# Kernel tuning notes

Hardware: AMD Instinct MI355X
Metric: run time of the kernel (lower is better)

Reference implementation:

```python
import jax, jax.numpy as jnp
import numpy as np

N_NODES = 50000
E_DIR = 250000
IN_FEATS = 256
N_HIDDEN = 64
N_CLASSES = 40
HEADS = 4
NEG_SLOPE = 0.2


def _build_graph():
    # mirrors to_undirected(edge_index) then add_self_loops(...)
    rng = np.random.default_rng(0)
    s = rng.integers(0, N_NODES, E_DIR)
    d = rng.integers(0, N_NODES, E_DIR)
    edges = np.stack([np.concatenate([s, d]), np.concatenate([d, s])], axis=0)
    edges = np.unique(edges, axis=1)  # dedup, as to_undirected does
    loops = np.arange(N_NODES)
    src = np.concatenate([edges[0], loops]).astype(np.int32)
    dst = np.concatenate([edges[1], loops]).astype(np.int32)
    return jnp.asarray(src), jnp.asarray(dst)


def setup_inputs() -> dict:
    key = jax.random.key(0)
    ks = jax.random.split(key, 16)
    src, dst = _build_graph()
    x = jax.random.uniform(ks[0], (N_NODES, IN_FEATS), dtype=jnp.float32)
    scale = 0.05
    # layer 0: IN -> HEADS*N_HIDDEN
    W0 = jax.random.normal(ks[1], (IN_FEATS, HEADS * N_HIDDEN), dtype=jnp.float32) * scale
    al0 = jax.random.normal(ks[2], (HEADS, N_HIDDEN), dtype=jnp.float32) * scale
    ar0 = jax.random.normal(ks[3], (HEADS, N_HIDDEN), dtype=jnp.float32) * scale
    b0 = jnp.zeros((HEADS * N_HIDDEN,), dtype=jnp.float32)
    # layer 1: HEADS*N_HIDDEN -> HEADS*N_HIDDEN
    W1 = jax.random.normal(ks[4], (HEADS * N_HIDDEN, HEADS * N_HIDDEN), dtype=jnp.float32) * scale
    al1 = jax.random.normal(ks[5], (HEADS, N_HIDDEN), dtype=jnp.float32) * scale
    ar1 = jax.random.normal(ks[6], (HEADS, N_HIDDEN), dtype=jnp.float32) * scale
    b1 = jnp.zeros((HEADS * N_HIDDEN,), dtype=jnp.float32)
    # layer 2: HEADS*N_HIDDEN -> HEADS*N_CLASSES (mean over heads at the end)
    W2 = jax.random.normal(ks[7], (HEADS * N_HIDDEN, HEADS * N_CLASSES), dtype=jnp.float32) * scale
    al2 = jax.random.normal(ks[8], (HEADS, N_CLASSES), dtype=jnp.float32) * scale
    ar2 = jax.random.normal(ks[9], (HEADS, N_CLASSES), dtype=jnp.float32) * scale
    b2 = jnp.zeros((HEADS * N_CLASSES,), dtype=jnp.float32)
    return {"x": x, "src": src, "dst": dst,
            "W0": W0, "al0": al0, "ar0": ar0, "b0": b0,
            "W1": W1, "al1": al1, "ar1": ar1, "b1": b1,
            "W2": W2, "al2": al2, "ar2": ar2, "b2": b2}


def _gat_layer(h, W, al, ar, b, src, dst):
    # DGL GATConv (no dropout, no residual): fc -> per-head attention -> edge softmax -> scatter-sum
    n = h.shape[0]
    nh, f = al.shape
    feat = (h @ W).reshape(n, nh, f)                      # [N,H,F]
    el = jnp.einsum('nhf,hf->nh', feat, al)               # [N,H]
    er = jnp.einsum('nhf,hf->nh', feat, ar)               # [N,H]
    e = jax.nn.leaky_relu(el[src] + er[dst], NEG_SLOPE)   # [E,H]
    emax = jax.lax.stop_gradient(jax.ops.segment_max(e, dst, num_segments=n))
    ee = jnp.exp(e - emax[dst])
    denom = jax.ops.segment_sum(ee, dst, num_segments=n)  # [N,H], >0 (self-loops)
    alpha = ee / denom[dst]                               # edge softmax over incoming edges
    msg = feat[src] * alpha[:, :, None]                   # [E,H,F]
    out = jax.ops.segment_sum(msg, dst, num_segments=n)   # [N,H,F]
    return out + b.reshape(1, nh, f)


def reference(x, src, dst, W0, al0, ar0, b0, W1, al1, ar1, b1, W2, al2, ar2, b2):
    n = x.shape[0]
    # x.shape[1] != 8189 -> row-normalize with clamp(min=1)
    h = x / jnp.clip(jnp.sum(x, axis=1, keepdims=True), 1.0)
    h = jax.nn.elu(_gat_layer(h, W0, al0, ar0, b0, src, dst)).reshape(n, -1)
    h = jax.nn.elu(_gat_layer(h, W1, al1, ar1, b1, src, dst)).reshape(n, -1)
    logits = _gat_layer(h, W2, al2, ar2, b2, src, dst).mean(axis=1)  # mean over heads
    return jax.nn.log_softmax(logits, axis=1)
```

## Files before the change

### kernel.cpp

```cpp
#include <hip/hip_runtime.h>
#include <math.h>

#define HEADS 4
#define HID 64
#define NCLS 40
#define IN_FEATS 256
#define NEG_SLOPE 0.2f
#define CAP 64
#define FP8_S 256.0f

typedef __attribute__((ext_vector_type(8))) short short8;
typedef __attribute__((ext_vector_type(4))) float floatx4;
typedef __attribute__((ext_vector_type(2))) float floatx2;

__device__ __forceinline__ ushort f2bf(float x) {
    union { float f; unsigned u; } v; v.f = x;
    unsigned r = (v.u + 0x7fff + ((v.u >> 16) & 1)) >> 16;
    return (ushort)r;
}
__device__ __forceinline__ unsigned char f2fp8(float x) {
    int pk = __builtin_amdgcn_cvt_pk_fp8_f32(x, x, 0, false);
    return (unsigned char)(pk & 0xff);
}
__device__ __forceinline__ void gload_lds16(const void* g, void* l) {
    __builtin_amdgcn_global_load_lds(
        (const __attribute__((address_space(1))) void*)g,
        (__attribute__((address_space(3))) void*)l, 16, 0, 0);
}

__global__ __launch_bounds__(256) void k_prep(const int* __restrict__ src,
                                              int* __restrict__ rowptr, int Em, int rb,
                                              const float* __restrict__ W0,
                                              const float* __restrict__ W1,
                                              const float* __restrict__ W2,
                                              ushort* __restrict__ Wt0,
                                              ushort* __restrict__ Wt1,
                                              ushort* __restrict__ Wt2,
                                              const float* __restrict__ al0,
                                              const float* __restrict__ ar0,
                                              const float* __restrict__ al1,
                                              const float* __restrict__ ar1,
                                              const float* __restrict__ al2,
                                              const float* __restrict__ ar2,
                                              ushort* __restrict__ Wel,
                                              const float* __restrict__ x,
                                              ushort* __restrict__ A16, int n) {
    int b = blockIdx.x;
    if (b < rb) {
        int j = b * 256 + threadIdx.x;
        if (j <= Em) {
            if (j == 0) {
                int hi = src[0];
                for (int v = 0; v <= hi; ++v) rowptr[v] = 0;
            } else if (j == Em) {
                int lo = src[Em - 1];
                for (int v = lo + 1; v <= n; ++v) rowptr[v] = Em;
            } else {
                int a = src[j - 1], c = src[j];
                for (int v = a + 1; v <= c; ++v) rowptr[v] = j;
            }
        }
        return;
    }
    b -= rb;
    if (b < 256) {
        int idx = b * 256 + threadIdx.x;
        int k = idx >> 8, c = idx & 255;
        Wt0[c * 256 + k] = f2bf(W0[idx]);
        Wt1[c * 256 + k] = f2bf(W1[idx]);
        if (idx < 40960) {
            int k2 = idx / 160, c2 = idx - k2 * 160;
            Wt2[c2 * 256 + k2] = f2bf(W2[idx]);
        }
        return;
    }
    b -= 256;
    if (b < 24) {
        int idx = b * 256 + threadIdx.x;
        int l = idx >> 11;
        int r = (idx >> 8) & 7;
        int k = idx & 255;
        int h = r & 3;
        bool isr = (r >= 4);
        const float* W  = (l == 0) ? W0 : (l == 1) ? W1 : W2;
        const float* av = isr ? ((l == 0) ? ar0 : (l == 1) ? ar1 : ar2)
                              : ((l == 0) ? al0 : (l == 1) ? al1 : al2);
        int F  = (l == 2) ? 40 : 64;
        int NC = (l == 2) ? 160 : 256;
        const float* wrow = W + (size_t)k * NC + h * F;
        const float* arow = av + h * F;
        float sum = 0.f;
        for (int f = 0; f < F; ++f) sum += wrow[f] * arow[f];
        Wel[idx] = f2bf(sum);
        return;
    }
    b -= 24;
    int row = b * 4 + (threadIdx.x >> 6);
    if (row >= n) return;
    int lane = threadIdx.x & 63;
    float4 v = reinterpret_cast<const float4*>(x + (size_t)row * 256)[lane];
    float s = v.x + v.y + v.z + v.w;
    for (int off = 32; off; off >>= 1) s += __shfl_down(s, off);
    s = __shfl(s, 0);
    float inv = 1.0f / fmaxf(s, 1.0f);
    ushort4 o;
    o.x = f2bf(v.x * inv); o.y = f2bf(v.y * inv);
    o.z = f2bf(v.z * inv); o.w = f2bf(v.w * inv);
    reinterpret_cast<ushort4*>(A16 + (size_t)row * 256)[lane] = o;
}

#define LDK 64
#define LDW 264

__global__ __launch_bounds__(256) void k_gemm_mfma(const ushort* __restrict__ A16,
                                                   const ushort* __restrict__ Wt,
                                                   const ushort* __restrict__ Welg,
                                                   unsigned char* __restrict__ Out8,
                                                   float* __restrict__ elv,
                                                   float* __restrict__ erv,
                                                   int n, int NCOL) {
    __shared__ ushort As[128 * LDK];
    __shared__ ushort Bs[128 * LDK];
    __shared__ ushort Wls[16 * LDW];
    int t = threadIdx.x;
    int lane = t & 63;
    int w = t >> 6;
    int wrow = (w & 1) * 64;
    int wcol = (w >> 1) * 64;
    int row0 = blockIdx.x * 128;
    int col0 = blockIdx.y * 128;
    int lrow = lane & 15;
    int kq = lane >> 4;
    bool fuse_blk = (blockIdx.y == 0);

    if (fuse_blk) {
        int r = t >> 5;
        int kk = (t & 31) * 8;
        uint4 v = *reinterpret_cast<const uint4*>(&Welg[r * 256 + kk]);
        *reinterpret_cast<uint4*>(&Wls[r * LDW + kk]) = v;
        *reinterpret_cast<uint4*>(&Wls[(r + 8) * LDW + kk]) = make_uint4(0u, 0u, 0u, 0u);
    }

    floatx4 acc[4][4];
    floatx4 acc_e[4];
#pragma unroll
    for (int i = 0; i < 4; ++i) {
        acc_e[i] = (floatx4)(0.f);
#pragma unroll
        for (int j = 0; j < 4; ++j) acc[i][j] = (floatx4)(0.f);
    }

    for (int k0 = 0; k0 < 256; k0 += 64) {
#pragma unroll
        for (int p = 0; p < 4; ++p) {
            int idx = p * 256 + t;
            int r = idx >> 3;
            int kk = (idx & 7) * 8;
            int gr = row0 + r; gr = (gr < n) ? gr : (n - 1);
            gload_lds16(&A16[(size_t)gr * 256 + k0 + kk], &As[idx * 8]);
        }
#pragma unroll
        for (int p = 0; p < 4; ++p) {
            int idx = p * 256 + t;
            int c = idx >> 3;
            int kk = (idx & 7) * 8;
            int gc = col0 + c; gc = (gc < NCOL) ? gc : (NCOL - 1);
            gload_lds16(&Wt[(size_t)gc * 256 + k0 + kk], &Bs[idx * 8]);
        }
        __syncthreads();

#pragma unroll
        for (int kc = 0; kc < 2; ++kc) {
            int kb = kc * 32 + kq * 8;
            short8 af[4], bf[4];
#pragma unroll
            for (int i = 0; i < 4; ++i)
                af[i] = *reinterpret_cast<const short8*>(&As[(wrow + 16 * i + lrow) * LDK + kb]);
#pragma unroll
            for (int j = 0; j < 4; ++j)
                bf[j] = *reinterpret_cast<const short8*>(&Bs[(wcol + 16 * j + lrow) * LDK + kb]);
#pragma unroll
            for (int i = 0; i < 4; ++i)
#pragma unroll
                for (int j = 0; j < 4; ++j)
                    acc[i][j] = __builtin_amdgcn_mfma_f32_16x16x32_bf16(af[i], bf[j], acc[i][j], 0, 0, 0);
            if (fuse_blk && wcol == 0) {
                short8 bw = *reinterpret_cast<const short8*>(&Wls[lrow * LDW + kb]);
#pragma unroll
                for (int i = 0; i < 4; ++i)
                    acc_e[i] = __builtin_amdgcn_mfma_f32_16x16x32_bf16(af[i], bw, acc_e[i], 0, 0, 0);
            }
        }
        __syncthreads();
    }

#pragma unroll
    for (int j = 0; j < 4; ++j) {
        int c = col0 + wcol + 16 * j + lrow;
        if (c >= NCOL) continue;
#pragma unroll
        for (int i = 0; i < 4; ++i) {
            int rbase = row0 + wrow + 16 * i + kq * 4;
#pragma unroll
            for (int r = 0; r < 4; ++r) {
                int gr = rbase + r;
                if (gr < n) Out8[(size_t)gr * NCOL + c] = f2fp8(acc[i][j][r] * FP8_S);
            }
        }
    }
    if (fuse_blk && wcol == 0 && lrow < 8) {
        bool is_er = (lrow >= 4);
        int h = lrow & 3;
#pragma unroll
        for (int i = 0; i < 4; ++i) {
            int rbase = row0 + wrow + 16 * i + kq * 4;
#pragma unroll
            for (int r = 0; r < 4; ++r) {
                int gr = rbase + r;
                if (gr < n) {
                    float v = acc_e[i][r];
                    if (is_er) erv[gr * 4 + h] = v;
                    else       elv[gr * 4 + h] = v;
                }
            }
        }
    }
}

template <int Fh, bool FINAL>
__global__ __launch_bounds__(256) void k_agg9(const unsigned char* __restrict__ F8,
                                              const float* __restrict__ el,
                                              const float* __restrict__ er,
                                              const int* __restrict__ rowptr,
                                              const int* __restrict__ dstv,
                                              const float* __restrict__ bias,
                                              ushort* __restrict__ out16,
                                              float* __restrict__ outF,
                                              int n) {
    constexpr int RL = 4 * Fh;
    constexpr bool FULL = (RL == 256);
    __shared__ float wls[4][CAP * 4];
    __shared__ int   mls[4][CAP];
    __shared__ float fbuf[4][FINAL ? 160 : 1];
    int wid = threadIdx.x >> 6;
    int node = blockIdx.x * 4 + wid;
    if (node >= n) node = n - 1;
    int lane = threadIdx.x & 63;
    int lo = rowptr[node];
    int deg_main = rowptr[node + 1] - lo;
    if (deg_main > CAP - 1) deg_main = CAP - 1;
    int deg = deg_main + 1;

    float* wl = wls[wid];
    int*   ml = mls[wid];

    int h = lane & 3;
    float ern = er[node * 4 + h];
    float wr[4];
    float s = 0.f;
    int ecount = 0;
    for (int e = lane >> 2; e < deg; e += 16) {
        int mid = (e < deg_main) ? dstv[lo + e] : node;
        if (h == 0) ml[e] = mid;
        float x = el[mid * 4 + h] + ern;
        x = (x > 0.f) ? x : NEG_SLOPE * x;
        float w = __expf(x);
        wr[ecount++] = w;
        s += w;
    }
#pragma unroll
    for (int off = 4; off < 64; off <<= 1) s += __shfl_xor(s, off);
    float invd = (1.0f / FP8_S) / s;
    {
        int e = lane >> 2;
        for (int i = 0; i < ecount; ++i, e += 16) wl[e * 4 + h] = wr[i] * invd;
    }
    asm volatile("s_waitcnt lgkmcnt(0)" ::: "memory");

    int my = 4 * lane;
    bool act = FULL || (my < RL);
    int hB = FULL ? (lane >> 4) : (my / Fh);
    float a0 = 0.f, a1 = 0.f, a2 = 0.f, a3 = 0.f;
#pragma unroll 4
    for (int j = 0; j < deg; ++j) {
        int mid = ml[j];
        float w = wl[j * 4 + hB];
        unsigned u = 0u;
        if (act) u = *reinterpret_cast<const unsigned*>(&F8[(size_t)mid * RL + my]);
        floatx2 p01 = __builtin_amdgcn_cvt_pk_f32_fp8(u, false);
        floatx2 p23 = __builtin_amdgcn_cvt_pk_f32_fp8(u, true);
        a0 = fmaf(w, p01.x, a0);
        a1 = fmaf(w, p01.y, a1);
        a2 = fmaf(w, p23.x, a2);
        a3 = fmaf(w, p23.y, a3);
    }

    if (!FINAL) {
        if (act) {
            float4 b4 = *reinterpret_cast<const float4*>(&bias[my]);
            float o0 = a0 + b4.x, o1 = a1 + b4.y, o2 = a2 + b4.z, o3 = a3 + b4.w;
            o0 = (o0 > 0.f) ? o0 : (__expf(o0) - 1.0f);
            o1 = (o1 > 0.f) ? o1 : (__expf(o1) - 1.0f);
            o2 = (o2 > 0.f) ? o2 : (__expf(o2) - 1.0f);
            o3 = (o3 > 0.f) ? o3 : (__expf(o3) - 1.0f);
            uint2 pk;
            pk.x = (unsigned)f2bf(o0) | ((unsigned)f2bf(o1) << 16);
            pk.y = (unsigned)f2bf(o2) | ((unsigned)f2bf(o3) << 16);
            *reinterpret_cast<uint2*>(&out16[(size_t)node * RL + my]) = pk;
        }
    } else {
        if (act) {
            float4 b4 = *reinterpret_cast<const float4*>(&bias[my]);
            fbuf[wid][my + 0] = a0 + b4.x;
            fbuf[wid][my + 1] = a1 + b4.y;
            fbuf[wid][my + 2] = a2 + b4.z;
            fbuf[wid][my + 3] = a3 + b4.w;
        }
        asm volatile("s_waitcnt lgkmcnt(0)" ::: "memory");
        float val = 0.f;
        if (lane < 40)
            val = 0.25f * (fbuf[wid][lane] + fbuf[wid][40 + lane] +
                           fbuf[wid][80 + lane] + fbuf[wid][120 + lane]);
        float mx = (lane < 40) ? val : -1e30f;
#pragma unroll
        for (int off = 32; off; off >>= 1) mx = fmaxf(mx, __shfl_xor(mx, off));
        float ex = (lane < 40) ? __expf(val - mx) : 0.f;
        float se = ex;
#pragma unroll
        for (int off = 32; off; off >>= 1) se += __shfl_xor(se, off);
        if (lane < 40) outF[(size_t)node * 40 + lane] = val - mx - logf(se);
    }
}

extern "C" void kernel_launch(void* const* d_in, const int* in_sizes, int n_in,
                              void* d_out, int out_size, void* d_ws, size_t ws_size,
                              hipStream_t stream) {
    const float* x  = (const float*)d_in[0];
    const int* src  = (const int*)d_in[1];
    const int* dst  = (const int*)d_in[2];
    const float* W0 = (const float*)d_in[3];
    const float* al0 = (const float*)d_in[4];
    const float* ar0 = (const float*)d_in[5];
    const float* b0 = (const float*)d_in[6];
    const float* W1 = (const float*)d_in[7];
    const float* al1 = (const float*)d_in[8];
    const float* ar1 = (const float*)d_in[9];
    const float* b1 = (const float*)d_in[10];
    const float* W2 = (const float*)d_in[11];
    const float* al2 = (const float*)d_in[12];
    const float* ar2 = (const float*)d_in[13];
    const float* b2 = (const float*)d_in[14];
    float* out = (float*)d_out;

    const int n = in_sizes[0] / IN_FEATS;
    const int E = in_sizes[1];
    const int Em = E - n;

    char* base = (char*)d_ws;
    size_t off = 0;
    auto alloc = [&](size_t bytes) {
        void* p = base + off;
        off = (off + bytes + 255) & ~(size_t)255;
        return p;
    };
    ushort* A16 = (ushort*)alloc((size_t)n * 256 * 2);
    unsigned char* F8 = (unsigned char*)alloc((size_t)n * 256);
    ushort* Wt0 = (ushort*)alloc((size_t)256 * 256 * 2);
    ushort* Wt1 = (ushort*)alloc((size_t)256 * 256 * 2);
    ushort* Wt2 = (ushort*)alloc((size_t)160 * 256 * 2);
    ushort* Wel = (ushort*)alloc((size_t)3 * 8 * 256 * 2);
    float* el  = (float*)alloc((size_t)n * HEADS * 4);
    float* er  = (float*)alloc((size_t)n * HEADS * 4);
    int* rowptr = (int*)alloc((size_t)(n + 1) * 4);
    (void)ws_size; (void)n_in; (void)out_size;

    const int rb = (Em + 1 + 255) / 256;
    const int nb4 = (n + 3) / 4;
    const int gemm_rows = (n + 127) / 128;

    k_prep<<<rb + 256 + 24 + nb4, 256, 0, stream>>>(src, rowptr, Em, rb,
                                                    W0, W1, W2, Wt0, Wt1, Wt2,
                                                    al0, ar0, al1, ar1, al2, ar2,
                                                    Wel, x, A16, n);

    k_gemm_mfma<<<dim3(gemm_rows, 2), 256, 0, stream>>>(A16, Wt0, Wel, F8, el, er, n, 256);
    k_agg9<HID, false><<<nb4, 256, 0, stream>>>(F8, el, er, rowptr, dst, b0, A16, out, n);

    k_gemm_mfma<<<dim3(gemm_rows, 2), 256, 0, stream>>>(A16, Wt1, Wel + 2048, F8, el, er, n, 256);
    k_agg9<HID, false><<<nb4, 256, 0, stream>>>(F8, el, er, rowptr, dst, b1, A16, out, n);

    k_gemm_mfma<<<dim3(gemm_rows, 2), 256, 0, stream>>>(A16, Wt2, Wel + 4096, F8, el, er, n, 160);
    k_agg9<NCLS, true><<<nb4, 256, 0, stream>>>(F8, el, er, rowptr, dst, b2, nullptr, out, n);
}
```

Baseline: 283.9 us.

## Fuse all GAT phases into one persistent kernel with grid-wide barriers

Replaces the seven separate launches (prep, three GEMMs, three aggregations) with a single persistent kernel. It sizes the grid from occupancy and uses grid-stride loops, with an atomic-counter barrier between phases. Shared memory is unioned across phases, and the el/er weight tile shrinks from 16 to 8 rows, with masked loads padding the rest. This removes launch overhead and inter-kernel gaps, at the cost of spin barriers and fewer resident blocks, which may lower latency hiding in the memory-bound aggregation. It also relies on every block being co-resident, since that is not guaranteed by a normal launch.

```diff
diff --git a/kernel.cpp b/kernel.cpp
--- a/kernel.cpp
+++ b/kernel.cpp
@@ -8,10 +8,16 @@
 #define NEG_SLOPE 0.2f
 #define CAP 64
 #define FP8_S 256.0f
+#define LDK 64
+#define LDW 264
 
 typedef __attribute__((ext_vector_type(8))) short short8;
 typedef __attribute__((ext_vector_type(4))) float floatx4;
 typedef __attribute__((ext_vector_type(2))) float floatx2;
+
+struct GemmS { ushort As[128 * LDK]; ushort Bs[128 * LDK]; ushort Wls[8 * LDW]; };
+struct AggS  { float wls[4][CAP * 4]; int mls[4][CAP]; float fbuf[4][160]; };
+union __align__(16) SharedU { GemmS g; AggS a; };
 
 __device__ __forceinline__ ushort f2bf(float x) {
     union { float f; unsigned u; } v; v.f = x;
@@ -28,308 +34,347 @@
         (__attribute__((address_space(3))) void*)l, 16, 0, 0);
 }
 
-__global__ __launch_bounds__(256) void k_prep(const int* __restrict__ src,
-                                              int* __restrict__ rowptr, int Em, int rb,
-                                              const float* __restrict__ W0,
-                                              const float* __restrict__ W1,
-                                              const float* __restrict__ W2,
-                                              ushort* __restrict__ Wt0,
-                                              ushort* __restrict__ Wt1,
-                                              ushort* __restrict__ Wt2,
-                                              const float* __restrict__ al0,
-                                              const float* __restrict__ ar0,
-                                              const float* __restrict__ al1,
-                                              const float* __restrict__ ar1,
-                                              const float* __restrict__ al2,
-                                              const float* __restrict__ ar2,
-                                              ushort* __restrict__ Wel,
-                                              const float* __restrict__ x,
-                                              ushort* __restrict__ A16, int n) {
-    int b = blockIdx.x;
-    if (b < rb) {
-        int j = b * 256 + threadIdx.x;
-        if (j <= Em) {
-            if (j == 0) {
-                int hi = src[0];
-                for (int v = 0; v <= hi; ++v) rowptr[v] = 0;
-            } else if (j == Em) {
-                int lo = src[Em - 1];
-                for (int v = lo + 1; v <= n; ++v) rowptr[v] = Em;
-            } else {
-                int a = src[j - 1], c = src[j];
-                for (int v = a + 1; v <= c; ++v) rowptr[v] = j;
-            }
-        }
-        return;
+__device__ __forceinline__ void gsync(int* cnt, int* gen) {
+    __syncthreads();
+    if (threadIdx.x == 0) {
+        int g = __hip_atomic_load(gen, __ATOMIC_RELAXED, __HIP_MEMORY_SCOPE_AGENT);
+        __threadfence();
+        int v = __hip_atomic_fetch_add(cnt, 1, __ATOMIC_ACQ_REL, __HIP_MEMORY_SCOPE_AGENT);
+        if (v == (int)gridDim.x - 1) {
+            __hip_atomic_store(cnt, 0, __ATOMIC_RELAXED, __HIP_MEMORY_SCOPE_AGENT);
+            __hip_atomic_fetch_add(gen, 1, __ATOMIC_RELEASE, __HIP_MEMORY_SCOPE_AGENT);
+        } else {
+            while (__hip_atomic_load(gen, __ATOMIC_ACQUIRE, __HIP_MEMORY_SCOPE_AGENT) == g)
+                __builtin_amdgcn_s_sleep(2);
+        }
+        __threadfence();
     }
-    b -= rb;
-    if (b < 256) {
-        int idx = b * 256 + threadIdx.x;
-        int k = idx >> 8, c = idx & 255;
-        Wt0[c * 256 + k] = f2bf(W0[idx]);
-        Wt1[c * 256 + k] = f2bf(W1[idx]);
-        if (idx < 40960) {
-            int k2 = idx / 160, c2 = idx - k2 * 160;
-            Wt2[c2 * 256 + k2] = f2bf(W2[idx]);
-        }
-        return;
-    }
-    b -= 256;
-    if (b < 24) {
-        int idx = b * 256 + threadIdx.x;
-        int l = idx >> 11;
-        int r = (idx >> 8) & 7;
-        int k = idx & 255;
-        int h = r & 3;
-        bool isr = (r >= 4);
-        const float* W  = (l == 0) ? W0 : (l == 1) ? W1 : W2;
-        const float* av = isr ? ((l == 0) ? ar0 : (l == 1) ? ar1 : ar2)
-                              : ((l == 0) ? al0 : (l == 1) ? al1 : al2);
-        int F  = (l == 2) ? 40 : 64;
-        int NC = (l == 2) ? 160 : 256;
-        const float* wrow = W + (size_t)k * NC + h * F;
-        const float* arow = av + h * F;
-        float sum = 0.f;
-        for (int f = 0; f < F; ++f) sum += wrow[f] * arow[f];
-        Wel[idx] = f2bf(sum);
-        return;
-    }
-    b -= 24;
-    int row = b * 4 + (threadIdx.x >> 6);
-    if (row >= n) return;
-    int lane = threadIdx.x & 63;
-    float4 v = reinterpret_cast<const float4*>(x + (size_t)row * 256)[lane];
-    float s = v.x + v.y + v.z + v.w;
-    for (int off = 32; off; off >>= 1) s += __shfl_down(s, off);
-    s = __shfl(s, 0);
-    float inv = 1.0f / fmaxf(s, 1.0f);
-    ushort4 o;
-    o.x = f2bf(v.x * inv); o.y = f2bf(v.y * inv);
-    o.z = f2bf(v.z * inv); o.w = f2bf(v.w * inv);
-    reinterpret_cast<ushort4*>(A16 + (size_t)row * 256)[lane] = o;
-}
-
-#define LDK 64
-#define LDW 264
-
-__global__ __launch_bounds__(256) void k_gemm_mfma(const ushort* __restrict__ A16,
-                                                   const ushort* __restrict__ Wt,
-                                                   const ushort* __restrict__ Welg,
-                                                   unsigned char* __restrict__ Out8,
-                                                   float* __restrict__ elv,
-                                                   float* __restrict__ erv,
-                                                   int n, int NCOL) {
-    __shared__ ushort As[128 * LDK];
-    __shared__ ushort Bs[128 * LDK];
-    __shared__ ushort Wls[16 * LDW];
+    __syncthreads();
+}
+
+__device__ __forceinline__ void phase_gemm(SharedU& sh,
+                                           const ushort* __restrict__ A16,
+                                           const ushort* __restrict__ Wt,
+                                           const ushort* __restrict__ Welg,
+                                           unsigned char* __restrict__ Out8,
+                                           float* __restrict__ elv,
+                                           float* __restrict__ erv,
+                                           int n, int NCOL, int ntile) {
     int t = threadIdx.x;
     int lane = t & 63;
     int w = t >> 6;
     int wrow = (w & 1) * 64;
     int wcol = (w >> 1) * 64;
-    int row0 = blockIdx.x * 128;
-    int col0 = blockIdx.y * 128;
     int lrow = lane & 15;
     int kq = lane >> 4;
-    bool fuse_blk = (blockIdx.y == 0);
-
-    if (fuse_blk) {
-        int r = t >> 5;
-        int kk = (t & 31) * 8;
-        uint4 v = *reinterpret_cast<const uint4*>(&Welg[r * 256 + kk]);
-        *reinterpret_cast<uint4*>(&Wls[r * LDW + kk]) = v;
-        *reinterpret_cast<uint4*>(&Wls[(r + 8) * LDW + kk]) = make_uint4(0u, 0u, 0u, 0u);
+
+    for (int tile = blockIdx.x; tile < ntile; tile += gridDim.x) {
+        int row0 = (tile >> 1) * 128;
+        int col0 = (tile & 1) * 128;
+        bool fuse_blk = (col0 == 0);
+
+        if (fuse_blk) {
+            int r = t >> 5;
+            int kk = (t & 31) * 8;
+            uint4 v = *reinterpret_cast<const uint4*>(&Welg[r * 256 + kk]);
+            *reinterpret_cast<uint4*>(&sh.g.Wls[r * LDW + kk]) = v;
+        }
+
+        floatx4 acc[4][4];
+        floatx4 acc_e[4];
+#pragma unroll
+        for (int i = 0; i < 4; ++i) {
+            acc_e[i] = (floatx4)(0.f);
+#pragma unroll
+            for (int j = 0; j < 4; ++j) acc[i][j] = (floatx4)(0.f);
+        }
+
+        for (int k0 = 0; k0 < 256; k0 += 64) {
+#pragma unroll
+            for (int p = 0; p < 4; ++p) {
+                int idx = p * 256 + t;
+                int r = idx >> 3;
+                int kk = (idx & 7) * 8;
+                int gr = row0 + r; gr = (gr < n) ? gr : (n - 1);
+                gload_lds16(&A16[(size_t)gr * 256 + k0 + kk], &sh.g.As[idx * 8]);
+            }
+#pragma unroll
+            for (int p = 0; p < 4; ++p) {
+                int idx = p * 256 + t;
+                int c = idx >> 3;
+                int kk = (idx & 7) * 8;
+                int gc = col0 + c; gc = (gc < NCOL) ? gc : (NCOL - 1);
+                gload_lds16(&Wt[(size_t)gc * 256 + k0 + kk], &sh.g.Bs[idx * 8]);
+            }
+            __syncthreads();
+
+#pragma unroll
+            for (int kc = 0; kc < 2; ++kc) {
+                int kb = kc * 32 + kq * 8;
+                short8 af[4], bf[4];
+#pragma unroll
+                for (int i = 0; i < 4; ++i)
+                    af[i] = *reinterpret_cast<const short8*>(&sh.g.As[(wrow + 16 * i + lrow) * LDK + kb]);
+#pragma unroll
+                for (int j = 0; j < 4; ++j)
+                    bf[j] = *reinterpret_cast<const short8*>(&sh.g.Bs[(wcol + 16 * j + lrow) * LDK + kb]);
+#pragma unroll
+                for (int i = 0; i < 4; ++i)
+#pragma unroll
+                    for (int j = 0; j < 4; ++j)
+                        acc[i][j] = __builtin_amdgcn_mfma_f32_16x16x32_bf16(af[i], bf[j], acc[i][j], 0, 0, 0);
+                if (fuse_blk && wcol == 0) {
+                    short8 bw = (short8)(short)0;
+                    if (lrow < 8)
+                        bw = *reinterpret_cast<const short8*>(&sh.g.Wls[lrow * LDW + kb]);
+#pragma unroll
+                    for (int i = 0; i < 4; ++i)
+                        acc_e[i] = __builtin_amdgcn_mfma_f32_16x16x32_bf16(af[i], bw, acc_e[i], 0, 0, 0);
+                }
+            }
+            __syncthreads();
+        }
+
+#pragma unroll
+        for (int j = 0; j < 4; ++j) {
+            int c = col0 + wcol + 16 * j + lrow;
+            if (c >= NCOL) continue;
+#pragma unroll
+            for (int i = 0; i < 4; ++i) {
+                int rbase = row0 + wrow + 16 * i + kq * 4;
+#pragma unroll
+                for (int r = 0; r < 4; ++r) {
+                    int gr = rbase + r;
+                    if (gr < n) Out8[(size_t)gr * NCOL + c] = f2fp8(acc[i][j][r] * FP8_S);
+                }
+            }
+        }
+        if (fuse_blk && wcol == 0 && lrow < 8) {
+            bool is_er = (lrow >= 4);
+            int h = lrow & 3;
+#pragma unroll
+            for (int i = 0; i < 4; ++i) {
+                int rbase = row0 + wrow + 16 * i + kq * 4;
+#pragma unroll
+                for (int r = 0; r < 4; ++r) {
+                    int gr = rbase + r;
+                    if (gr < n) {
+                        float v = acc_e[i][r];
+                        if (is_er) erv[gr * 4 + h] = v;
+                        else       elv[gr * 4 + h] = v;
+                    }
+                }
+            }
+        }
     }
-
-    floatx4 acc[4][4];
-    floatx4 acc_e[4];
-#pragma unroll
-    for (int i = 0; i < 4; ++i) {
-        acc_e[i] = (floatx4)(0.f);
-#pragma unroll
-        for (int j = 0; j < 4; ++j) acc[i][j] = (floatx4)(0.f);
-    }
-
-    for (int k0 = 0; k0 < 256; k0 += 64) {
-#pragma unroll
-        for (int p = 0; p < 4; ++p) {
-            int idx = p * 256 + t;
-            int r = idx >> 3;
-            int kk = (idx & 7) * 8;
-            int gr = row0 + r; gr = (gr < n) ? gr : (n - 1);
-            gload_lds16(&A16[(size_t)gr * 256 + k0 + kk], &As[idx * 8]);
-        }
-#pragma unroll
-        for (int p = 0; p < 4; ++p) {
-            int idx = p * 256 + t;
-            int c = idx >> 3;
-            int kk = (idx & 7) * 8;
-            int gc = col0 + c; gc = (gc < NCOL) ? gc : (NCOL - 1);
-            gload_lds16(&Wt[(size_t)gc * 256 + k0 + kk], &Bs[idx * 8]);
-        }
-        __syncthreads();
-
-#pragma unroll
-        for (int kc = 0; kc < 2; ++kc) {
-            int kb = kc * 32 + kq * 8;
-            short8 af[4], bf[4];
-#pragma unroll
-            for (int i = 0; i < 4; ++i)
-                af[i] = *reinterpret_cast<const short8*>(&As[(wrow + 16 * i + lrow) * LDK + kb]);
-#pragma unroll
-            for (int j = 0; j < 4; ++j)
-                bf[j] = *reinterpret_cast<const short8*>(&Bs[(wcol + 16 * j + lrow) * LDK + kb]);
-#pragma unroll
-            for (int i = 0; i < 4; ++i)
-#pragma unroll
-                for (int j = 0; j < 4; ++j)
-                    acc[i][j] = __builtin_amdgcn_mfma_f32_16x16x32_bf16(af[i], bf[j], acc[i][j], 0, 0, 0);
-            if (fuse_blk && wcol == 0) {
-                short8 bw = *reinterpret_cast<const short8*>(&Wls[lrow * LDW + kb]);
-#pragma unroll
-                for (int i = 0; i < 4; ++i)
-                    acc_e[i] = __builtin_amdgcn_mfma_f32_16x16x32_bf16(af[i], bw, acc_e[i], 0, 0, 0);
-            }
-        }
-        __syncthreads();
-    }
-
-#pragma unroll
-    for (int j = 0; j < 4; ++j) {
-        int c = col0 + wcol + 16 * j + lrow;
-        if (c >= NCOL) continue;
-#pragma unroll
-        for (int i = 0; i < 4; ++i) {
-            int rbase = row0 + wrow + 16 * i + kq * 4;
-#pragma unroll
-            for (int r = 0; r < 4; ++r) {
-                int gr = rbase + r;
-                if (gr < n) Out8[(size_t)gr * NCOL + c] = f2fp8(acc[i][j][r] * FP8_S);
-            }
-        }
-    }
-    if (fuse_blk && wcol == 0 && lrow < 8) {
-        bool is_er = (lrow >= 4);
-        int h = lrow & 3;
-#pragma unroll
-        for (int i = 0; i < 4; ++i) {
-            int rbase = row0 + wrow + 16 * i + kq * 4;
-#pragma unroll
-            for (int r = 0; r < 4; ++r) {
-                int gr = rbase + r;
-                if (gr < n) {
-                    float v = acc_e[i][r];
-                    if (is_er) erv[gr * 4 + h] = v;
-                    else       elv[gr * 4 + h] = v;
-                }
-            }
-        }
-    }
 }
 
 template <int Fh, bool FINAL>
-__global__ __launch_bounds__(256) void k_agg9(const unsigned char* __restrict__ F8,
-                                              const float* __restrict__ el,
-                                              const float* __restrict__ er,
-                                              const int* __restrict__ rowptr,
-                                              const int* __restrict__ dstv,
-                                              const float* __restrict__ bias,
-                                              ushort* __restrict__ out16,
-                                              float* __restrict__ outF,
-                                              int n) {
+__device__ __forceinline__ void phase_agg(SharedU& sh,
+                                          const unsigned char* __restrict__ F8,
+                                          const float* __restrict__ el,
+                                          const float* __restrict__ er,
+                                          const int* __restrict__ rowptr,
+                                          const int* __restrict__ dstv,
+                                          const float* __restrict__ bias,
+                                          ushort* __restrict__ out16,
+                                          float* __restrict__ outF,
+                                          int n, int nb4) {
     constexpr int RL = 4 * Fh;
     constexpr bool FULL = (RL == 256);
-    __shared__ float wls[4][CAP * 4];
-    __shared__ int   mls[4][CAP];
-    __shared__ float fbuf[4][FINAL ? 160 : 1];
     int wid = threadIdx.x >> 6;
-    int node = blockIdx.x * 4 + wid;
-    if (node >= n) node = n - 1;
     int lane = threadIdx.x & 63;
-    int lo = rowptr[node];
-    int deg_main = rowptr[node + 1] - lo;
-    if (deg_main > CAP - 1) deg_main = CAP - 1;
-    int deg = deg_main + 1;
-
-    float* wl = wls[wid];
-    int*   ml = mls[wid];
-
-    int h = lane & 3;
-    float ern = er[node * 4 + h];
-    float wr[4];
-    float s = 0.f;
-    int ecount = 0;
-    for (int e = lane >> 2; e < deg; e += 16) {
-        int mid = (e < deg_main) ? dstv[lo + e] : node;
-        if (h == 0) ml[e] = mid;
-        float x = el[mid * 4 + h] + ern;
-        x = (x > 0.f) ? x : NEG_SLOPE * x;
-        float w = __expf(x);
-        wr[ecount++] = w;
-        s += w;
+    float* wl = sh.a.wls[wid];
+    int*   ml = sh.a.mls[wid];
+
+    for (int gblk = blockIdx.x; gblk < nb4; gblk += gridDim.x) {
+        int node = gblk * 4 + wid;
+        if (node >= n) node = n - 1;
+        int lo = rowptr[node];
+        int deg_main = rowptr[node + 1] - lo;
+        if (deg_main > CAP - 1) deg_main = CAP - 1;
+        int deg = deg_main + 1;
+
+        int h = lane & 3;
+        float ern = er[node * 4 + h];
+        float wr[4];
+        float s = 0.f;
+        int ecount = 0;
+        for (int e = lane >> 2; e < deg; e += 16) {
+            int mid = (e < deg_main) ? dstv[lo + e] : node;
+            if (h == 0) ml[e] = mid;
+            float xv = el[mid * 4 + h] + ern;
+            xv = (xv > 0.f) ? xv : NEG_SLOPE * xv;
+            float wv = __expf(xv);
+            wr[ecount++] = wv;
+            s += wv;
+        }
+#pragma unroll
+        for (int off = 4; off < 64; off <<= 1) s += __shfl_xor(s, off);
+        float invd = (1.0f / FP8_S) / s;
+        {
+            int e = lane >> 2;
+            for (int i = 0; i < ecount; ++i, e += 16) wl[e * 4 + h] = wr[i] * invd;
+        }
+        asm volatile("s_waitcnt lgkmcnt(0)" ::: "memory");
+
+        int my = 4 * lane;
+        bool act = FULL || (my < RL);
+        int hB = FULL ? (lane >> 4) : (my / Fh);
+        float a0 = 0.f, a1 = 0.f, a2 = 0.f, a3 = 0.f;
+#pragma unroll 4
+        for (int j = 0; j < deg; ++j) {
+            int mid = ml[j];
+            float wv = wl[j * 4 + hB];
+            unsigned u = 0u;
+            if (act) u = *reinterpret_cast<const unsigned*>(&F8[(size_t)mid * RL + my]);
+            floatx2 p01 = __builtin_amdgcn_cvt_pk_f32_fp8(u, false);
+            floatx2 p23 = __builtin_amdgcn_cvt_pk_f32_fp8(u, true);
+            a0 = fmaf(wv, p01.x, a0);
+            a1 = fmaf(wv, p01.y, a1);
+            a2 = fmaf(wv, p23.x, a2);
+            a3 = fmaf(wv, p23.y, a3);
+        }
+
+        if (!FINAL) {
+            if (act) {
+                float4 b4 = *reinterpret_cast<const float4*>(&bias[my]);
+                float o0 = a0 + b4.x, o1 = a1 + b4.y, o2 = a2 + b4.z, o3 = a3 + b4.w;
+                o0 = (o0 > 0.f) ? o0 : (__expf(o0) - 1.0f);
+                o1 = (o1 > 0.f) ? o1 : (__expf(o1) - 1.0f);
+                o2 = (o2 > 0.f) ? o2 : (__expf(o2) - 1.0f);
+                o3 = (o3 > 0.f) ? o3 : (__expf(o3) - 1.0f);
+                uint2 pk;
+                pk.x = (unsigned)f2bf(o0) | ((unsigned)f2bf(o1) << 16);
+                pk.y = (unsigned)f2bf(o2) | ((unsigned)f2bf(o3) << 16);
+                *reinterpret_cast<uint2*>(&out16[(size_t)node * RL + my]) = pk;
+            }
+        } else {
+            if (act) {
+                float4 b4 = *reinterpret_cast<const float4*>(&bias[my]);
+                sh.a.fbuf[wid][my + 0] = a0 + b4.x;
+                sh.a.fbuf[wid][my + 1] = a1 + b4.y;
+                sh.a.fbuf[wid][my + 2] = a2 + b4.z;
+                sh.a.fbuf[wid][my + 3] = a3 + b4.w;
+            }
+            asm volatile("s_waitcnt lgkmcnt(0)" ::: "memory");
+            float val = 0.f;
+            if (lane < 40)
+                val = 0.25f * (sh.a.fbuf[wid][lane] + sh.a.fbuf[wid][40 + lane] +
+                               sh.a.fbuf[wid][80 + lane] + sh.a.fbuf[wid][120 + lane]);
+            float mx = (lane < 40) ? val : -1e30f;
+#pragma unroll
+            for (int off = 32; off; off >>= 1) mx = fmaxf(mx, __shfl_xor(mx, off));
+            float ex = (lane < 40) ? __expf(val - mx) : 0.f;
+            float se = ex;
+#pragma unroll
+            for (int off = 32; off; off >>= 1) se += __shfl_xor(se, off);
+            if (lane < 40) outF[(size_t)node * 40 + lane] = val - mx - logf(se);
+        }
     }
-#pragma unroll
-    for (int off = 4; off < 64; off <<= 1) s += __shfl_xor(s, off);
-    float invd = (1.0f / FP8_S) / s;
+}
+
+__global__ __launch_bounds__(256) void k_mega(
+        const int* __restrict__ src, const int* __restrict__ dstv,
+        const float* __restrict__ x,
+        const float* __restrict__ W0, const float* __restrict__ W1,
+        const float* __restrict__ W2,
+        const float* __restrict__ al0, const float* __restrict__ ar0,
+        const float* __restrict__ al1, const float* __restrict__ ar1,
+        const float* __restrict__ al2, const float* __restrict__ ar2,
+        const float* __restrict__ bias0, const float* __restrict__ bias1,
+        const float* __restrict__ bias2,
+        ushort* __restrict__ Wt0, ushort* __restrict__ Wt1,
+        ushort* __restrict__ Wt2,
+        ushort* __restrict__ Wel, ushort* __restrict__ A16,
+        unsigned char* __restrict__ F8,
+        float* __restrict__ el, float* __restrict__ er,
+        int* __restrict__ rowptr, float* __restrict__ out,
+        int n, int Em, int rb, int nb4, int ntile,
+        int* cnt, int* gen) {
+    __shared__ SharedU sh;
+    int t = threadIdx.x;
+
     {
-        int e = lane >> 2;
-        for (int i = 0; i < ecount; ++i, e += 16) wl[e * 4 + h] = wr[i] * invd;
+        int TOTP = rb + 256 + 24 + ((n + 3) >> 2);
+        for (int bv = blockIdx.x; bv < TOTP; bv += gridDim.x) {
+            int b = bv;
+            if (b < rb) {
+                int j = b * 256 + t;
+                if (j <= Em) {
+                    if (j == 0) {
+                        int hi = src[0];
+                        for (int v = 0; v <= hi; ++v) rowptr[v] = 0;
+                    } else if (j == Em) {
+                        int lo = src[Em - 1];
+                        for (int v = lo + 1; v <= n; ++v) rowptr[v] = Em;
+                    } else {
+                        int a = src[j - 1], c = src[j];
+                        for (int v = a + 1; v <= c; ++v) rowptr[v] = j;
+                    }
+                }
+                continue;
+            }
+            b -= rb;
+            if (b < 256) {
+                int idx = b * 256 + t;
+                int k = idx >> 8, c = idx & 255;
+                Wt0[c * 256 + k] = f2bf(W0[idx]);
+                Wt1[c * 256 + k] = f2bf(W1[idx]);
+                if (idx < 40960) {
+                    int k2 = idx / 160, c2 = idx - k2 * 160;
+                    Wt2[c2 * 256 + k2] = f2bf(W2[idx]);
+                }
+                continue;
+            }
+            b -= 256;
+            if (b < 24) {
+                int idx = b * 256 + t;
+                int l = idx >> 11;
+                int r = (idx >> 8) & 7;
+                int k = idx & 255;
+                int h = r & 3;
+                bool isr = (r >= 4);
+                const float* W  = (l == 0) ? W0 : (l == 1) ? W1 : W2;
+                const float* av = isr ? ((l == 0) ? ar0 : (l == 1) ? ar1 : ar2)
+                                      : ((l == 0) ? al0 : (l == 1) ? al1 : al2);
+                int F  = (l == 2) ? 40 : 64;
+                int NC = (l == 2) ? 160 : 256;
+                const float* wrow = W + (size_t)k * NC + h * F;
+                const float* arow = av + h * F;
+                float sum = 0.f;
+                for (int f = 0; f < F; ++f) sum += wrow[f] * arow[f];
+                Wel[idx] = f2bf(sum);
+                continue;
+            }
+            b -= 24;
+            int row = b * 4 + (t >> 6);
+            if (row < n) {
+                int lane = t & 63;
+                float4 v = reinterpret_cast<const float4*>(x + (size_t)row * 256)[lane];
+                float s = v.x + v.y + v.z + v.w;
+                for (int off = 32; off; off >>= 1) s += __shfl_down(s, off);
+                s = __shfl(s, 0);
+                float inv = 1.0f / fmaxf(s, 1.0f);
+                ushort4 o;
+                o.x = f2bf(v.x * inv); o.y = f2bf(v.y * inv);
+                o.z = f2bf(v.z * inv); o.w = f2bf(v.w * inv);
+                reinterpret_cast<ushort4*>(A16 + (size_t)row * 256)[lane] = o;
+            }
+        }
     }
-    asm volatile("s_waitcnt lgkmcnt(0)" ::: "memory");
-
-    int my = 4 * lane;
-    bool act = FULL || (my < RL);
-    int hB = FULL ? (lane >> 4) : (my / Fh);
-    float a0 = 0.f, a1 = 0.f, a2 = 0.f, a3 = 0.f;
-#pragma unroll 4
-    for (int j = 0; j < deg; ++j) {
-        int mid = ml[j];
-        float w = wl[j * 4 + hB];
-        unsigned u = 0u;
-        if (act) u = *reinterpret_cast<const unsigned*>(&F8[(size_t)mid * RL + my]);
-        floatx2 p01 = __builtin_amdgcn_cvt_pk_f32_fp8(u, false);
-        floatx2 p23 = __builtin_amdgcn_cvt_pk_f32_fp8(u, true);
-        a0 = fmaf(w, p01.x, a0);
-        a1 = fmaf(w, p01.y, a1);
-        a2 = fmaf(w, p23.x, a2);
-        a3 = fmaf(w, p23.y, a3);
-    }
-
-    if (!FINAL) {
-        if (act) {
-            float4 b4 = *reinterpret_cast<const float4*>(&bias[my]);
-            float o0 = a0 + b4.x, o1 = a1 + b4.y, o2 = a2 + b4.z, o3 = a3 + b4.w;
-            o0 = (o0 > 0.f) ? o0 : (__expf(o0) - 1.0f);
-            o1 = (o1 > 0.f) ? o1 : (__expf(o1) - 1.0f);
-            o2 = (o2 > 0.f) ? o2 : (__expf(o2) - 1.0f);
-            o3 = (o3 > 0.f) ? o3 : (__expf(o3) - 1.0f);
-            uint2 pk;
-            pk.x = (unsigned)f2bf(o0) | ((unsigned)f2bf(o1) << 16);
-            pk.y = (unsigned)f2bf(o2) | ((unsigned)f2bf(o3) << 16);
-            *reinterpret_cast<uint2*>(&out16[(size_t)node * RL + my]) = pk;
-        }
-    } else {
-        if (act) {
-            float4 b4 = *reinterpret_cast<const float4*>(&bias[my]);
-            fbuf[wid][my + 0] = a0 + b4.x;
-            fbuf[wid][my + 1] = a1 + b4.y;
-            fbuf[wid][my + 2] = a2 + b4.z;
-            fbuf[wid][my + 3] = a3 + b4.w;
-        }
-        asm volatile("s_waitcnt lgkmcnt(0)" ::: "memory");
-        float val = 0.f;
-        if (lane < 40)
-            val = 0.25f * (fbuf[wid][lane] + fbuf[wid][40 + lane] +
-                           fbuf[wid][80 + lane] + fbuf[wid][120 + lane]);
-        float mx = (lane < 40) ? val : -1e30f;
-#pragma unroll
-        for (int off = 32; off; off >>= 1) mx = fmaxf(mx, __shfl_xor(mx, off));
-        float ex = (lane < 40) ? __expf(val - mx) : 0.f;
-        float se = ex;
-#pragma unroll
-        for (int off = 32; off; off >>= 1) se += __shfl_xor(se, off);
-        if (lane < 40) outF[(size_t)node * 40 + lane] = val - mx - logf(se);
-    }
+    gsync(cnt, gen);
+    phase_gemm(sh, A16, Wt0, Wel, F8, el, er, n, 256, ntile);
+    gsync(cnt, gen);
+    phase_agg<HID, false>(sh, F8, el, er, rowptr, dstv, bias0, A16, nullptr, n, nb4);
+    gsync(cnt, gen);
+    phase_gemm(sh, A16, Wt1, Wel + 2048, F8, el, er, n, 256, ntile);
+    gsync(cnt, gen);
+    phase_agg<HID, false>(sh, F8, el, er, rowptr, dstv, bias1, A16, nullptr, n, nb4);
+    gsync(cnt, gen);
+    phase_gemm(sh, A16, Wt2, Wel + 4096, F8, el, er, n, 160, ntile);
+    gsync(cnt, gen);
+    phase_agg<NCLS, true>(sh, F8, el, er, rowptr, dstv, bias2, nullptr, out, n, nb4);
 }
 
 extern "C" void kernel_launch(void* const* d_in, const int* in_sizes, int n_in,
@@ -372,23 +417,28 @@
     float* el  = (float*)alloc((size_t)n * HEADS * 4);
     float* er  = (float*)alloc((size_t)n * HEADS * 4);
     int* rowptr = (int*)alloc((size_t)(n + 1) * 4);
+    int* bar = (int*)alloc(256);
     (void)ws_size; (void)n_in; (void)out_size;
 
     const int rb = (Em + 1 + 255) / 256;
     const int nb4 = (n + 3) / 4;
-    const int gemm_rows = (n + 127) / 128;
-
-    k_prep<<<rb + 256 + 24 + nb4, 256, 0, stream>>>(src, rowptr, Em, rb,
-                                                    W0, W1, W2, Wt0, Wt1, Wt2,
-                                                    al0, ar0, al1, ar1, al2, ar2,
-                                                    Wel, x, A16, n);
-
-    k_gemm_mfma<<<dim3(gemm_rows, 2), 256, 0, stream>>>(A16, Wt0, Wel, F8, el, er, n, 256);
-    k_agg9<HID, false><<<nb4, 256, 0, stream>>>(F8, el, er, rowptr, dst, b0, A16, out, n);
-
-    k_gemm_mfma<<<dim3(gemm_rows, 2), 256, 0, stream>>>(A16, Wt1, Wel + 2048, F8, el, er, n, 256);
-    k_agg9<HID, false><<<nb4, 256, 0, stream>>>(F8, el, er, rowptr, dst, b1, A16, out, n);
-
-    k_gemm_mfma<<<dim3(gemm_rows, 2), 256, 0, stream>>>(A16, Wt2, Wel + 4096, F8, el, er, n, 160);
-    k_agg9<NCLS, true><<<nb4, 256, 0, stream>>>(F8, el, er, rowptr, dst, b2, nullptr, out, n);
-}
+    const int ntile = 2 * ((n + 127) / 128);
+
+    hipMemsetAsync(bar, 0, 8, stream);
+
+    int bpc = 0;
+    if (hipOccupancyMaxActiveBlocksPerMultiprocessor(&bpc, k_mega, 256, 0) != hipSuccess
+        || bpc < 1) bpc = 2;
+    if (bpc > 4) bpc = 4;
+    int nblk = bpc * 256;
+
+    k_mega<<<nblk, 256, 0, stream>>>(src, dst, x,
+                                     W0, W1, W2,
+                                     al0, ar0, al1, ar1, al2, ar2,
+                                     b0, b1, b2,
+                                     Wt0, Wt1, Wt2,
+                                     Wel, A16, F8, el, er,
+                                     rowptr, out,
+                                     n, Em, rb, nb4, ntile,
+                                     bar, bar + 1);
+}
```

New measurement: 1.025 ms. 3.61x slower.

## Double-buffer GEMM LDS tiles, keep el/er weights in registers, XCD-aware tile mapping

Applied to the files above, without the earlier changes.

Rewrites the MFMA GEMM main loop as a fully unrolled two-buffer pipeline: the next K-slice is loaded asynchronously into LDS while the current one is computed, with partial vmcnt waits replacing full barriers. The attention-projection weight slice moves from LDS into registers. A 1D grid is remapped so consecutive tiles (both column halves of a row block) land on the same XCD for L2 reuse. This doubles LDS use per block and adds register pressure, which may lower occupancy.

```diff
diff --git a/kernel.cpp b/kernel.cpp
--- a/kernel.cpp
+++ b/kernel.cpp
@@ -8,6 +8,7 @@
 #define NEG_SLOPE 0.2f
 #define CAP 64
 #define FP8_S 256.0f
+#define LDK 64
 
 typedef __attribute__((ext_vector_type(8))) short short8;
 typedef __attribute__((ext_vector_type(4))) float floatx4;
@@ -109,8 +110,28 @@
     reinterpret_cast<ushort4*>(A16 + (size_t)row * 256)[lane] = o;
 }
 
-#define LDK 64
-#define LDW 264
+__device__ __forceinline__ void stage_tile(const ushort* __restrict__ A16,
+                                           const ushort* __restrict__ Wt,
+                                           ushort* As, ushort* Bs,
+                                           int t, int row0, int col0, int k0,
+                                           int n, int NCOL) {
+#pragma unroll
+    for (int p = 0; p < 4; ++p) {
+        int idx = p * 256 + t;
+        int r = idx >> 3;
+        int kk = (idx & 7) * 8;
+        int gr = row0 + r; gr = (gr < n) ? gr : (n - 1);
+        gload_lds16(&A16[(size_t)gr * 256 + k0 + kk], &As[idx * 8]);
+    }
+#pragma unroll
+    for (int p = 0; p < 4; ++p) {
+        int idx = p * 256 + t;
+        int c = idx >> 3;
+        int kk = (idx & 7) * 8;
+        int gc = col0 + c; gc = (gc < NCOL) ? gc : (NCOL - 1);
+        gload_lds16(&Wt[(size_t)gc * 256 + k0 + kk], &Bs[idx * 8]);
+    }
+}
 
 __global__ __launch_bounds__(256) void k_gemm_mfma(const ushort* __restrict__ A16,
                                                    const ushort* __restrict__ Wt,
@@ -118,28 +139,39 @@
                                                    unsigned char* __restrict__ Out8,
                                                    float* __restrict__ elv,
                                                    float* __restrict__ erv,
-                                                   int n, int NCOL) {
-    __shared__ ushort As[128 * LDK];
-    __shared__ ushort Bs[128 * LDK];
-    __shared__ ushort Wls[16 * LDW];
+                                                   int n, int NCOL, int ntile) {
+    __shared__ ushort As[2][128 * LDK];
+    __shared__ ushort Bs[2][128 * LDK];
     int t = threadIdx.x;
     int lane = t & 63;
     int w = t >> 6;
     int wrow = (w & 1) * 64;
     int wcol = (w >> 1) * 64;
-    int row0 = blockIdx.x * 128;
-    int col0 = blockIdx.y * 128;
     int lrow = lane & 15;
     int kq = lane >> 4;
-    bool fuse_blk = (blockIdx.y == 0);
-
-    if (fuse_blk) {
-        int r = t >> 5;
-        int kk = (t & 31) * 8;
-        uint4 v = *reinterpret_cast<const uint4*>(&Welg[r * 256 + kk]);
-        *reinterpret_cast<uint4*>(&Wls[r * LDW + kk]) = v;
-        *reinterpret_cast<uint4*>(&Wls[(r + 8) * LDW + kk]) = make_uint4(0u, 0u, 0u, 0u);
-    }
+
+    int tile;
+    {
+        int q = ntile >> 3, r = ntile & 7;
+        int xcd = blockIdx.x & 7, pos = blockIdx.x >> 3;
+        tile = (xcd < r ? xcd * (q + 1) : r * (q + 1) + (xcd - r) * q) + pos;
+    }
+    int row0 = (tile >> 1) * 128;
+    int col0 = (tile & 1) * 128;
+    bool fuse_blk = (col0 == 0);
+    bool fuse_w = fuse_blk && (wcol == 0);
+
+    short8 bwr[4][2];
+#pragma unroll
+    for (int s4 = 0; s4 < 4; ++s4)
+#pragma unroll
+        for (int kc = 0; kc < 2; ++kc) {
+            if (fuse_w && lrow < 8)
+                bwr[s4][kc] = *reinterpret_cast<const short8*>(
+                    &Welg[lrow * 256 + s4 * 64 + kc * 32 + kq * 8]);
+            else
+                bwr[s4][kc] = (short8)(short)0;
+        }
 
     floatx4 acc[4][4];
     floatx4 acc_e[4];
@@ -150,49 +182,58 @@
         for (int j = 0; j < 4; ++j) acc[i][j] = (floatx4)(0.f);
     }
 
-    for (int k0 = 0; k0 < 256; k0 += 64) {
-#pragma unroll
-        for (int p = 0; p < 4; ++p) {
-            int idx = p * 256 + t;
-            int r = idx >> 3;
-            int kk = (idx & 7) * 8;
-            int gr = row0 + r; gr = (gr < n) ? gr : (n - 1);
-            gload_lds16(&A16[(size_t)gr * 256 + k0 + kk], &As[idx * 8]);
-        }
-#pragma unroll
-        for (int p = 0; p < 4; ++p) {
-            int idx = p * 256 + t;
-            int c = idx >> 3;
-            int kk = (idx & 7) * 8;
-            int gc = col0 + c; gc = (gc < NCOL) ? gc : (NCOL - 1);
-            gload_lds16(&Wt[(size_t)gc * 256 + k0 + kk], &Bs[idx * 8]);
-        }
-        __syncthreads();
-
-#pragma unroll
-        for (int kc = 0; kc < 2; ++kc) {
-            int kb = kc * 32 + kq * 8;
-            short8 af[4], bf[4];
-#pragma unroll
-            for (int i = 0; i < 4; ++i)
-                af[i] = *reinterpret_cast<const short8*>(&As[(wrow + 16 * i + lrow) * LDK + kb]);
-#pragma unroll
-            for (int j = 0; j < 4; ++j)
-                bf[j] = *reinterpret_cast<const short8*>(&Bs[(wcol + 16 * j + lrow) * LDK + kb]);
-#pragma unroll
-            for (int i = 0; i < 4; ++i)
-#pragma unroll
-                for (int j = 0; j < 4; ++j)
-                    acc[i][j] = __builtin_amdgcn_mfma_f32_16x16x32_bf16(af[i], bf[j], acc[i][j], 0, 0, 0);
-            if (fuse_blk && wcol == 0) {
-                short8 bw = *reinterpret_cast<const short8*>(&Wls[lrow * LDW + kb]);
-#pragma unroll
-                for (int i = 0; i < 4; ++i)
-                    acc_e[i] = __builtin_amdgcn_mfma_f32_16x16x32_bf16(af[i], bw, acc_e[i], 0, 0, 0);
-            }
-        }
-        __syncthreads();
-    }
+    stage_tile(A16, Wt, As[0], Bs[0], t, row0, col0, 0, n, NCOL);
+    stage_tile(A16, Wt, As[1], Bs[1], t, row0, col0, 64, n, NCOL);
+
+#define GEMM_COMPUTE(BUF, S4)                                                         \
+    {                                                                                 \
+        _Pragma("unroll")                                                             \
+        for (int kc = 0; kc < 2; ++kc) {                                              \
+            int kb = kc * 32 + kq * 8;                                                \
+            short8 af[4], bf[4];                                                      \
+            _Pragma("unroll")                                                         \
+            for (int i = 0; i < 4; ++i)                                               \
+                af[i] = *reinterpret_cast<const short8*>(                             \
+                    &As[BUF][(wrow + 16 * i + lrow) * LDK + kb]);                     \
+            _Pragma("unroll")                                                         \
+            for (int j = 0; j < 4; ++j)                                               \
+                bf[j] = *reinterpret_cast<const short8*>(                             \
+                    &Bs[BUF][(wcol + 16 * j + lrow) * LDK + kb]);                     \
+            _Pragma("unroll")                                                         \
+            for (int i = 0; i < 4; ++i)                                               \
+                _Pragma("unroll")                                                     \
+                for (int j = 0; j < 4; ++j)                                           \
+                    acc[i][j] = __builtin_amdgcn_mfma_f32_16x16x32_bf16(              \
+                        af[i], bf[j], acc[i][j], 0, 0, 0);                            \
+            if (fuse_w) {                                                             \
+                _Pragma("unroll")                                                     \
+                for (int i = 0; i < 4; ++i)                                           \
+                    acc_e[i] = __builtin_amdgcn_mfma_f32_16x16x32_bf16(               \
+                        af[i], bwr[S4][kc], acc_e[i], 0, 0, 0);                       \
+            }                                                                         \
+        }                                                                             \
+    }
+
+    asm volatile("s_waitcnt vmcnt(8)" ::: "memory");
+    __builtin_amdgcn_s_barrier();
+    GEMM_COMPUTE(0, 0)
+    __builtin_amdgcn_s_barrier();
+    stage_tile(A16, Wt, As[0], Bs[0], t, row0, col0, 128, n, NCOL);
+
+    asm volatile("s_waitcnt vmcnt(8)" ::: "memory");
+    __builtin_amdgcn_s_barrier();
+    GEMM_COMPUTE(1, 1)
+    __builtin_amdgcn_s_barrier();
+    stage_tile(A16, Wt, As[1], Bs[1], t, row0, col0, 192, n, NCOL);
+
+    asm volatile("s_waitcnt vmcnt(8)" ::: "memory");
+    __builtin_amdgcn_s_barrier();
+    GEMM_COMPUTE(0, 2)
+    __builtin_amdgcn_s_barrier();
+
+    asm volatile("s_waitcnt vmcnt(0)" ::: "memory");
+    __builtin_amdgcn_s_barrier();
+    GEMM_COMPUTE(1, 3)
 
 #pragma unroll
     for (int j = 0; j < 4; ++j) {
@@ -208,7 +249,7 @@
             }
         }
     }
-    if (fuse_blk && wcol == 0 && lrow < 8) {
+    if (fuse_w && lrow < 8) {
         bool is_er = (lrow >= 4);
         int h = lrow & 3;
 #pragma unroll
@@ -376,19 +417,19 @@
 
     const int rb = (Em + 1 + 255) / 256;
     const int nb4 = (n + 3) / 4;
-    const int gemm_rows = (n + 127) / 128;
+    const int ntile = 2 * ((n + 127) / 128);
 
     k_prep<<<rb + 256 + 24 + nb4, 256, 0, stream>>>(src, rowptr, Em, rb,
                                                     W0, W1, W2, Wt0, Wt1, Wt2,
                                                     al0, ar0, al1, ar1, al2, ar2,
                                                     Wel, x, A16, n);
 
-    k_gemm_mfma<<<dim3(gemm_rows, 2), 256, 0, stream>>>(A16, Wt0, Wel, F8, el, er, n, 256);
+    k_gemm_mfma<<<ntile, 256, 0, stream>>>(A16, Wt0, Wel, F8, el, er, n, 256, ntile);
     k_agg9<HID, false><<<nb4, 256, 0, stream>>>(F8, el, er, rowptr, dst, b0, A16, out, n);
 
-    k_gemm_mfma<<<dim3(gemm_rows, 2), 256, 0, stream>>>(A16, Wt1, Wel + 2048, F8, el, er, n, 256);
+    k_gemm_mfma<<<ntile, 256, 0, stream>>>(A16, Wt1, Wel + 2048, F8, el, er, n, 256, ntile);
     k_agg9<HID, false><<<nb4, 256, 0, stream>>>(F8, el, er, rowptr, dst, b1, A16, out, n);
 
-    k_gemm_mfma<<<dim3(gemm_rows, 2), 256, 0, stream>>>(A16, Wt2, Wel + 4096, F8, el, er, n, 160);
+    k_gemm_mfma<<<ntile, 256, 0, stream>>>(A16, Wt2, Wel + 4096, F8, el, er, n, 160, ntile);
     k_agg9<NCLS, true><<<nb4, 256, 0, stream>>>(F8, el, er, rowptr, dst, b2, nullptr, out, n);
 }
```

After: 286.6 us. Within noise of the previous version (+1.0%).
